# Kernel tuning notes

Measured on AMD Instinct MI355X. Metric: run time of the kernel, lower is better.

Reference implementation:

```python
import jax, jax.numpy as jnp
import numpy as np

BATCH = 1024
MAX_LEN = 200
MAX_K = 8
IN_U = 256
OUT_U = 256
ITERATION = 3
NEG_PAD = jnp.float32(-2.0**16 + 1)  # -65535, same as torch code


def squash(x):
    # NOTE: torch code sums over dim=1, which here is the capsule (max_K) axis.
    vec_sq_norm = jnp.sum(jnp.square(x), axis=1, keepdims=True)
    scale = vec_sq_norm / (1.0 + vec_sq_norm) / jnp.sqrt(vec_sq_norm + 1e-9)
    return scale * x


def setup_inputs() -> dict:
    key = jax.random.key(0)
    k1, k2, k3, k4 = jax.random.split(key, 4)
    low_capsule = jax.random.normal(k1, (BATCH, MAX_LEN, IN_U), dtype=jnp.float32)
    seq_len = jax.random.randint(k2, (BATCH, 1), 0, MAX_LEN)  # values < max_len per assert
    S_matrix = jax.random.normal(k3, (IN_U, OUT_U), dtype=jnp.float32)
    B_matrix = jax.random.normal(k4, (1, MAX_K, MAX_LEN), dtype=jnp.float32)
    return {"low_capsule": low_capsule, "S_matrix": S_matrix,
            "B_matrix": B_matrix, "seq_len": seq_len}


def reference(low_capsule, S_matrix, B_matrix, seq_len):
    # mask: [B,1,L], broadcasts against B_matrix [1,K,L] -> [B,K,L]
    mask = jnp.arange(MAX_LEN)[None, None, :] < seq_len[:, :, None]
    # loop-invariant projection (torch recomputes identically each iteration)
    low_new = jnp.einsum('ble,eo->blo', low_capsule, S_matrix)  # [B,L,O]
    Bm = B_matrix
    high = None
    for _ in range(ITERATION):
        logits = jnp.where(mask, Bm, NEG_PAD)          # [B,K,L]
        W = jax.nn.softmax(logits, axis=-1)            # [B,K,L]
        high = squash(jnp.einsum('bkl,blo->bko', W, low_new))  # [B,K,O]
        B_delta = jnp.sum(jnp.einsum('bko,blo->bkl', high, low_new),
                          axis=0, keepdims=True)       # [1,K,L]
        Bm = Bm + B_delta
    return high
```

## Files before the change

### kernel.cpp

```cpp
#include <hip/hip_runtime.h>

#define BATCH   1024
#define MAXLEN  200
#define KCAPS   8
#define INU     256
#define OUTU    256
#define NEGPAD  -65535.0f
#define HSTR    264

typedef _Float16 f16;
typedef _Float16 f16x8 __attribute__((ext_vector_type(8)));
typedef float    f32x4 __attribute__((ext_vector_type(4)));
typedef float    f32x2 __attribute__((ext_vector_type(2)));

__global__ void k_prep(const float* __restrict__ S, const float* __restrict__ Bm,
                       f16* __restrict__ Shi, f16* __restrict__ Slo,
                       f16* __restrict__ Thi, f16* __restrict__ Tlo,
                       float* __restrict__ Bcur) {
    int idx = blockIdx.x * 256 + threadIdx.x;
    if (idx < KCAPS * MAXLEN) Bcur[idx] = Bm[idx];
    int j    = idx & 7;
    int lane = (idx >> 3) & 63;
    int nf   = (idx >> 9) & 15;
    int ks   = idx >> 13;
    int k = ks * 32 + (lane >> 4) * 8 + j;
    int n = nf * 16 + (lane & 15);
    float vS = S[k * 256 + n];
    f16 hS = (f16)vS;
    Shi[idx] = hS;
    Slo[idx] = (f16)(vS - (float)hS);
    float vT = S[n * 256 + k];
    f16 hT = (f16)vT;
    Thi[idx] = hT;
    Tlo[idx] = (f16)(vT - (float)hT);
}

#define EFRAG(MF, ACC) do {                                                          \
    const int l_  = (MF) * 16 + r15;                                                 \
    const int lc_ = (l_ < MAXLEN) ? l_ : (MAXLEN - 1);                               \
    const float* ap_ = lb + (size_t)lc_ * INU + q * 8;                               \
    f32x4 va[8], vb[8];                                                              \
    _Pragma("unroll")                                                                \
    for (int ks = 0; ks < 8; ks++) {                                                 \
        va[ks] = *reinterpret_cast<const f32x4*>(ap_ + ks * 32);                     \
        vb[ks] = *reinterpret_cast<const f32x4*>(ap_ + ks * 32 + 4);                 \
    }                                                                                \
    _Pragma("unroll")                                                                \
    for (int ks = 0; ks < 8; ks++) {                                                 \
        const int ob_ = ks * 32 + q * 8;                                             \
        f32x4 h0 = *reinterpret_cast<const f32x4*>(&GH[r15 * HSTR + ob_]);           \
        f32x4 h1 = *reinterpret_cast<const f32x4*>(&GH[r15 * HSTR + ob_ + 4]);       \
        f16x8 bh, bl, ah, al;                                                        \
        _Pragma("unroll")                                                            \
        for (int j = 0; j < 4; j++) { f16 t = (f16)h0[j]; bh[j] = t; bl[j] = (f16)(h0[j] - (float)t); } \
        _Pragma("unroll")                                                            \
        for (int j = 0; j < 4; j++) { f16 t = (f16)h1[j]; bh[4+j] = t; bl[4+j] = (f16)(h1[j] - (float)t); } \
        _Pragma("unroll")                                                            \
        for (int j = 0; j < 4; j++) { f16 t = (f16)va[ks][j]; ah[j] = t; al[j] = (f16)(va[ks][j] - (float)t); } \
        _Pragma("unroll")                                                            \
        for (int j = 0; j < 4; j++) { f16 t = (f16)vb[ks][j]; ah[4+j] = t; al[4+j] = (f16)(vb[ks][j] - (float)t); } \
        ACC = __builtin_amdgcn_mfma_f32_16x16x32_f16(ah, bh, ACC, 0, 0, 0);          \
        ACC = __builtin_amdgcn_mfma_f32_16x16x32_f16(al, bh, ACC, 0, 0, 0);          \
        ACC = __builtin_amdgcn_mfma_f32_16x16x32_f16(ah, bl, ACC, 0, 0, 0);          \
    }                                                                                \
} while (0)

__global__ __launch_bounds__(512, 4) void k_G(const float* __restrict__ Bcur,
                                              const int*   __restrict__ seq_len,
                                              const float* __restrict__ low,
                                              const f16*   __restrict__ Shi,
                                              const f16*   __restrict__ Slo,
                                              const f16*   __restrict__ Thi,
                                              const f16*   __restrict__ Tlo,
                                              float*       __restrict__ partials,
                                              float*       __restrict__ out,
                                              int do_T) {
    __shared__ float Wl[KCAPS * MAXLEN];
    __shared__ float GH[16 * HSTR];
    __shared__ float Sl2[2 * KCAPS * 256];
    const int b   = blockIdx.x;
    const int tid = threadIdx.x;
    const int len = seq_len[b];

    for (int i = tid; i < KCAPS * MAXLEN; i += 512) Wl[i] = Bcur[i];
    for (int i = tid; i < 16 * HSTR; i += 512) GH[i] = 0.f;
    __syncthreads();

    {
        const int k  = tid >> 6;
        const int ln = tid & 63;
        float m = -3.4e38f;
        for (int l = ln; l < MAXLEN; l += 64) {
            float v = (l < len) ? Wl[k * MAXLEN + l] : NEGPAD;
            m = fmaxf(m, v);
        }
        #pragma unroll
        for (int off = 32; off >= 1; off >>= 1) m = fmaxf(m, __shfl_xor(m, off));
        float ssum = 0.f;
        for (int l = ln; l < MAXLEN; l += 64) {
            float v = (l < len) ? Wl[k * MAXLEN + l] : NEGPAD;
            ssum += __expf(v - m);
        }
        #pragma unroll
        for (int off = 32; off >= 1; off >>= 1) ssum += __shfl_xor(ssum, off);
        float inv = 1.f / ssum;
        for (int l = ln; l < MAXLEN; l += 64) {
            float v = (l < len) ? Wl[k * MAXLEN + l] : NEGPAD;
            Wl[k * MAXLEN + l] = __expf(v - m) * inv;
        }
    }
    __syncthreads();

    const float* lb = low + (size_t)b * (MAXLEN * INU);

    {
        const int cp = tid & 127;
        const int rg = tid >> 7;
        const int lim = (len == 0) ? MAXLEN : len;
        const float* cb = lb + cp * 2;
        f32x2 g[KCAPS];
        #pragma unroll
        for (int k = 0; k < KCAPS; k++) g[k] = (f32x2){0.f, 0.f};
        int l = rg;
        for (; l + 4 < lim; l += 8) {
            f32x2 va = *reinterpret_cast<const f32x2*>(cb + l * INU);
            f32x2 vb = *reinterpret_cast<const f32x2*>(cb + (l + 4) * INU);
            #pragma unroll
            for (int k = 0; k < KCAPS; k++) {
                float wa = Wl[k * MAXLEN + l];
                float wb = Wl[k * MAXLEN + l + 4];
                g[k][0] = fmaf(wa, va[0], g[k][0]);
                g[k][1] = fmaf(wa, va[1], g[k][1]);
                g[k][0] = fmaf(wb, vb[0], g[k][0]);
                g[k][1] = fmaf(wb, vb[1], g[k][1]);
            }
        }
        if (l < lim) {
            f32x2 va = *reinterpret_cast<const f32x2*>(cb + l * INU);
            #pragma unroll
            for (int k = 0; k < KCAPS; k++) {
                float wa = Wl[k * MAXLEN + l];
                g[k][0] = fmaf(wa, va[0], g[k][0]);
                g[k][1] = fmaf(wa, va[1], g[k][1]);
            }
        }
        if (rg >= 2) {
            #pragma unroll
            for (int k = 0; k < KCAPS; k++)
                *reinterpret_cast<f32x2*>(&Sl2[((rg - 2) * KCAPS + k) * 256 + cp * 2]) = g[k];
        }
        __syncthreads();
        if (rg == 1) {
            #pragma unroll
            for (int k = 0; k < KCAPS; k++) {
                f32x2 t = *reinterpret_cast<f32x2*>(&Sl2[(KCAPS + k) * 256 + cp * 2]);
                g[k][0] += t[0]; g[k][1] += t[1];
                *reinterpret_cast<f32x2*>(&Sl2[(KCAPS + k) * 256 + cp * 2]) = g[k];
            }
        } else if (rg == 0) {
            #pragma unroll
            for (int k = 0; k < KCAPS; k++) {
                f32x2 t = *reinterpret_cast<f32x2*>(&Sl2[k * 256 + cp * 2]);
                g[k][0] += t[0]; g[k][1] += t[1];
            }
        }
        __syncthreads();
        if (rg == 0) {
            #pragma unroll
            for (int k = 0; k < KCAPS; k++) {
                f32x2 t = *reinterpret_cast<f32x2*>(&Sl2[(KCAPS + k) * 256 + cp * 2]);
                GH[k * HSTR + cp * 2]     = g[k][0] + t[0];
                GH[k * HSTR + cp * 2 + 1] = g[k][1] + t[1];
            }
        }
    }
    __syncthreads();

    const int wv = tid >> 6, lane = tid & 63;
    const int r15 = lane & 15, q = lane >> 4;
    f32x4 aC[2];
    aC[0] = (f32x4){0.f, 0.f, 0.f, 0.f};
    aC[1] = (f32x4){0.f, 0.f, 0.f, 0.f};
    #pragma unroll
    for (int ks = 0; ks < 8; ks++) {
        const float* gp = &GH[r15 * HSTR + ks * 32 + q * 8];
        f32x4 a0 = *reinterpret_cast<const f32x4*>(gp);
        f32x4 a1 = *reinterpret_cast<const f32x4*>(gp + 4);
        f16x8 ah, al;
        #pragma unroll
        for (int j = 0; j < 4; j++) {
            f16 t = (f16)a0[j]; ah[j] = t; al[j] = (f16)(a0[j] - (float)t);
        }
        #pragma unroll
        for (int j = 0; j < 4; j++) {
            f16 t = (f16)a1[j]; ah[4 + j] = t; al[4 + j] = (f16)(a1[j] - (float)t);
        }
        #pragma unroll
        for (int i = 0; i < 2; i++) {
            const int nf = wv * 2 + i;
            f16x8 bh = *reinterpret_cast<const f16x8*>(Shi + (ks * 16 + nf) * 512 + lane * 8);
            f16x8 bl = *reinterpret_cast<const f16x8*>(Slo + (ks * 16 + nf) * 512 + lane * 8);
            aC[i] = __builtin_amdgcn_mfma_f32_16x16x32_f16(ah, bh, aC[i], 0, 0, 0);
            aC[i] = __builtin_amdgcn_mfma_f32_16x16x32_f16(al, bh, aC[i], 0, 0, 0);
            aC[i] = __builtin_amdgcn_mfma_f32_16x16x32_f16(ah, bl, aC[i], 0, 0, 0);
        }
    }
    float s0, s1;
    {
        float n0 = aC[0][0]*aC[0][0] + aC[0][1]*aC[0][1] + aC[0][2]*aC[0][2] + aC[0][3]*aC[0][3];
        float n1 = aC[1][0]*aC[1][0] + aC[1][1]*aC[1][1] + aC[1][2]*aC[1][2] + aC[1][3]*aC[1][3];
        n0 += __shfl_xor(n0, 16);
        n1 += __shfl_xor(n1, 16);
        s0 = n0 / (1.f + n0) * (1.f / sqrtf(n0 + 1e-9f));
        s1 = n1 / (1.f + n1) * (1.f / sqrtf(n1 + 1e-9f));
    }
    if (!do_T) {
        if (q < 2) {
            #pragma unroll
            for (int r = 0; r < 4; r++) {
                out[((size_t)b * KCAPS + q * 4 + r) * OUTU + (wv * 2 + 0) * 16 + r15] = s0 * aC[0][r];
                out[((size_t)b * KCAPS + q * 4 + r) * OUTU + (wv * 2 + 1) * 16 + r15] = s1 * aC[1][r];
            }
        }
        return;
    }
    __syncthreads();
    if (q < 2) {
        #pragma unroll
        for (int r = 0; r < 4; r++) {
            GH[(q * 4 + r) * HSTR + (wv * 2 + 0) * 16 + r15] = s0 * aC[0][r];
            GH[(q * 4 + r) * HSTR + (wv * 2 + 1) * 16 + r15] = s1 * aC[1][r];
        }
    }
    __syncthreads();

    f32x4 aD[2];
    aD[0] = (f32x4){0.f, 0.f, 0.f, 0.f};
    aD[1] = (f32x4){0.f, 0.f, 0.f, 0.f};
    #pragma unroll
    for (int ks = 0; ks < 8; ks++) {
        const float* hp = &GH[r15 * HSTR + ks * 32 + q * 8];
        f32x4 a0 = *reinterpret_cast<const f32x4*>(hp);
        f32x4 a1 = *reinterpret_cast<const f32x4*>(hp + 4);
        f16x8 ah, al;
        #pragma unroll
        for (int j = 0; j < 4; j++) {
            f16 t = (f16)a0[j]; ah[j] = t; al[j] = (f16)(a0[j] - (float)t);
        }
        #pragma unroll
        for (int j = 0; j < 4; j++) {
            f16 t = (f16)a1[j]; ah[4 + j] = t; al[4 + j] = (f16)(a1[j] - (float)t);
        }
        #pragma unroll
        for (int i = 0; i < 2; i++) {
            const int nf = wv * 2 + i;
            f16x8 bh = *reinterpret_cast<const f16x8*>(Thi + (ks * 16 + nf) * 512 + lane * 8);
            f16x8 bl = *reinterpret_cast<const f16x8*>(Tlo + (ks * 16 + nf) * 512 + lane * 8);
            aD[i] = __builtin_amdgcn_mfma_f32_16x16x32_f16(ah, bh, aD[i], 0, 0, 0);
            aD[i] = __builtin_amdgcn_mfma_f32_16x16x32_f16(al, bh, aD[i], 0, 0, 0);
            aD[i] = __builtin_amdgcn_mfma_f32_16x16x32_f16(ah, bl, aD[i], 0, 0, 0);
        }
    }
    __syncthreads();
    if (q < 2) {
        #pragma unroll
        for (int r = 0; r < 4; r++) {
            GH[(q * 4 + r) * HSTR + (wv * 2 + 0) * 16 + r15] = aD[0][r];
            GH[(q * 4 + r) * HSTR + (wv * 2 + 1) * 16 + r15] = aD[1][r];
        }
    }
    __syncthreads();

    f32x4 accA = (f32x4){0.f, 0.f, 0.f, 0.f};
    f32x4 accB = (f32x4){0.f, 0.f, 0.f, 0.f};
    EFRAG(wv, accA);
    if (wv < 5) EFRAG(wv + 8, accB);

    if (r15 < KCAPS) {
        const int kcol = r15;
        {
            const int lbase = wv * 16 + q * 4;
            #pragma unroll
            for (int r = 0; r < 4; r++)
                partials[(size_t)(kcol * MAXLEN + lbase + r) * BATCH + b] = accA[r];
        }
        if (wv < 5) {
            const int lbase = (wv + 8) * 16 + q * 4;
            #pragma unroll
            for (int r = 0; r < 4; r++) {
                const int l = lbase + r;
                if (l < MAXLEN)
                    partials[(size_t)(kcol * MAXLEN + l) * BATCH + b] = accB[r];
            }
        }
    }
}

__global__ __launch_bounds__(256) void k_update(const float* __restrict__ partials,
                                                float* __restrict__ Bcur) {
    __shared__ float red[256];
    const int i   = blockIdx.x;
    const int tid = threadIdx.x;
    float s = 0.f;
    #pragma unroll
    for (int j = 0; j < BATCH / 256; j++) s += partials[(size_t)i * BATCH + tid + j * 256];
    red[tid] = s;
    __syncthreads();
    for (int st = 128; st > 0; st >>= 1) {
        if (tid < st) red[tid] += red[tid + st];
        __syncthreads();
    }
    if (tid == 0) Bcur[i] += red[0];
}

extern "C" void kernel_launch(void* const* d_in, const int* in_sizes, int n_in,
                              void* d_out, int out_size, void* d_ws, size_t ws_size,
                              hipStream_t stream) {
    const float* low = (const float*)d_in[0];
    const float* S   = (const float*)d_in[1];
    const float* Bm  = (const float*)d_in[2];
    const int*   seq = (const int*)d_in[3];
    float* out = (float*)d_out;

    char* ws = (char*)d_ws;
    float* Bcur     = (float*)ws;
    float* partials = (float*)(ws + 6400);
    f16*   Shi      = (f16*)(ws + 6560000);
    f16*   Slo      = (f16*)(ws + 6691072);
    f16*   Thi      = (f16*)(ws + 6822144);
    f16*   Tlo      = (f16*)(ws + 6953216);

    k_prep<<<256, 256, 0, stream>>>(S, Bm, Shi, Slo, Thi, Tlo, Bcur);
    for (int it = 0; it < 3; it++) {
        int last = (it == 2);
        k_G<<<BATCH, 512, 0, stream>>>(Bcur, seq, low, Shi, Slo, Thi, Tlo,
                                       partials, out, last ? 0 : 1);
        if (!last) k_update<<<KCAPS * MAXLEN, 256, 0, stream>>>(partials, Bcur);
    }
}
```

Measured before the change: 227.7 us.

## Shrink k_G to 256 threads with four waves each covering more columns

Halves the k_G block from 512 to 256 threads, so each wave now handles four N-fragments in the S/T MFMA products and up to four L-fragments in the E stage. The weighted-sum stage is rewritten so each wave streams full rows as float4 with a software-prefetched next row, and partial sums are reduced through the GH shared buffer instead of a separate Sl2 array, which cuts shared memory. The EFRAG macro loads inputs in two halves to lower register pressure, and the cross-lane-group reduction is now done with shuffles. The intent is to raise occupancy and per-thread work while cutting LDS and barrier cost, at the price of fewer threads per block available to hide memory latency.

New measurement: 328.9 us. 1.44x slower.

```diff
diff --git a/kernel.cpp b/kernel.cpp
--- a/kernel.cpp
+++ b/kernel.cpp
@@ -11,7 +11,6 @@
 typedef _Float16 f16;
 typedef _Float16 f16x8 __attribute__((ext_vector_type(8)));
 typedef float    f32x4 __attribute__((ext_vector_type(4)));
-typedef float    f32x2 __attribute__((ext_vector_type(2)));
 
 __global__ void k_prep(const float* __restrict__ S, const float* __restrict__ Bm,
                        f16* __restrict__ Shi, f16* __restrict__ Slo,
@@ -39,33 +38,36 @@
     const int l_  = (MF) * 16 + r15;                                                 \
     const int lc_ = (l_ < MAXLEN) ? l_ : (MAXLEN - 1);                               \
     const float* ap_ = lb + (size_t)lc_ * INU + q * 8;                               \
-    f32x4 va[8], vb[8];                                                              \
     _Pragma("unroll")                                                                \
-    for (int ks = 0; ks < 8; ks++) {                                                 \
-        va[ks] = *reinterpret_cast<const f32x4*>(ap_ + ks * 32);                     \
-        vb[ks] = *reinterpret_cast<const f32x4*>(ap_ + ks * 32 + 4);                 \
-    }                                                                                \
-    _Pragma("unroll")                                                                \
-    for (int ks = 0; ks < 8; ks++) {                                                 \
-        const int ob_ = ks * 32 + q * 8;                                             \
-        f32x4 h0 = *reinterpret_cast<const f32x4*>(&GH[r15 * HSTR + ob_]);           \
-        f32x4 h1 = *reinterpret_cast<const f32x4*>(&GH[r15 * HSTR + ob_ + 4]);       \
-        f16x8 bh, bl, ah, al;                                                        \
+    for (int half = 0; half < 2; half++) {                                           \
+        f32x4 va[4], vb[4];                                                          \
         _Pragma("unroll")                                                            \
-        for (int j = 0; j < 4; j++) { f16 t = (f16)h0[j]; bh[j] = t; bl[j] = (f16)(h0[j] - (float)t); } \
+        for (int kk = 0; kk < 4; kk++) {                                             \
+            va[kk] = *reinterpret_cast<const f32x4*>(ap_ + (half * 4 + kk) * 32);    \
+            vb[kk] = *reinterpret_cast<const f32x4*>(ap_ + (half * 4 + kk) * 32 + 4);\
+        }                                                                            \
         _Pragma("unroll")                                                            \
-        for (int j = 0; j < 4; j++) { f16 t = (f16)h1[j]; bh[4+j] = t; bl[4+j] = (f16)(h1[j] - (float)t); } \
-        _Pragma("unroll")                                                            \
-        for (int j = 0; j < 4; j++) { f16 t = (f16)va[ks][j]; ah[j] = t; al[j] = (f16)(va[ks][j] - (float)t); } \
-        _Pragma("unroll")                                                            \
-        for (int j = 0; j < 4; j++) { f16 t = (f16)vb[ks][j]; ah[4+j] = t; al[4+j] = (f16)(vb[ks][j] - (float)t); } \
-        ACC = __builtin_amdgcn_mfma_f32_16x16x32_f16(ah, bh, ACC, 0, 0, 0);          \
-        ACC = __builtin_amdgcn_mfma_f32_16x16x32_f16(al, bh, ACC, 0, 0, 0);          \
-        ACC = __builtin_amdgcn_mfma_f32_16x16x32_f16(ah, bl, ACC, 0, 0, 0);          \
+        for (int kk = 0; kk < 4; kk++) {                                             \
+            const int ob_ = (half * 4 + kk) * 32 + q * 8;                            \
+            f32x4 h0 = *reinterpret_cast<const f32x4*>(&GH[r15 * HSTR + ob_]);       \
+            f32x4 h1 = *reinterpret_cast<const f32x4*>(&GH[r15 * HSTR + ob_ + 4]);   \
+            f16x8 bh, bl, ah, al;                                                    \
+            _Pragma("unroll")                                                        \
+            for (int j = 0; j < 4; j++) { f16 t = (f16)h0[j]; bh[j] = t; bl[j] = (f16)(h0[j] - (float)t); } \
+            _Pragma("unroll")                                                        \
+            for (int j = 0; j < 4; j++) { f16 t = (f16)h1[j]; bh[4+j] = t; bl[4+j] = (f16)(h1[j] - (float)t); } \
+            _Pragma("unroll")                                                        \
+            for (int j = 0; j < 4; j++) { f16 t = (f16)va[kk][j]; ah[j] = t; al[j] = (f16)(va[kk][j] - (float)t); } \
+            _Pragma("unroll")                                                        \
+            for (int j = 0; j < 4; j++) { f16 t = (f16)vb[kk][j]; ah[4+j] = t; al[4+j] = (f16)(vb[kk][j] - (float)t); } \
+            ACC = __builtin_amdgcn_mfma_f32_16x16x32_f16(ah, bh, ACC, 0, 0, 0);      \
+            ACC = __builtin_amdgcn_mfma_f32_16x16x32_f16(al, bh, ACC, 0, 0, 0);      \
+            ACC = __builtin_amdgcn_mfma_f32_16x16x32_f16(ah, bl, ACC, 0, 0, 0);      \
+        }                                                                            \
     }                                                                                \
 } while (0)
 
-__global__ __launch_bounds__(512, 4) void k_G(const float* __restrict__ Bcur,
+__global__ __launch_bounds__(256, 6) void k_G(const float* __restrict__ Bcur,
                                               const int*   __restrict__ seq_len,
                                               const float* __restrict__ low,
                                               const f16*   __restrict__ Shi,
@@ -77,34 +79,33 @@
                                               int do_T) {
     __shared__ float Wl[KCAPS * MAXLEN];
     __shared__ float GH[16 * HSTR];
-    __shared__ float Sl2[2 * KCAPS * 256];
     const int b   = blockIdx.x;
     const int tid = threadIdx.x;
     const int len = seq_len[b];
 
-    for (int i = tid; i < KCAPS * MAXLEN; i += 512) Wl[i] = Bcur[i];
-    for (int i = tid; i < 16 * HSTR; i += 512) GH[i] = 0.f;
+    for (int i = tid; i < KCAPS * MAXLEN; i += 256) Wl[i] = Bcur[i];
+    for (int i = tid; i < 16 * HSTR; i += 256) GH[i] = 0.f;
     __syncthreads();
 
     {
-        const int k  = tid >> 6;
-        const int ln = tid & 63;
+        const int k  = tid >> 5;
+        const int ln = tid & 31;
         float m = -3.4e38f;
-        for (int l = ln; l < MAXLEN; l += 64) {
+        for (int l = ln; l < MAXLEN; l += 32) {
             float v = (l < len) ? Wl[k * MAXLEN + l] : NEGPAD;
             m = fmaxf(m, v);
         }
         #pragma unroll
-        for (int off = 32; off >= 1; off >>= 1) m = fmaxf(m, __shfl_xor(m, off));
+        for (int off = 16; off >= 1; off >>= 1) m = fmaxf(m, __shfl_xor(m, off));
         float ssum = 0.f;
-        for (int l = ln; l < MAXLEN; l += 64) {
+        for (int l = ln; l < MAXLEN; l += 32) {
             float v = (l < len) ? Wl[k * MAXLEN + l] : NEGPAD;
             ssum += __expf(v - m);
         }
         #pragma unroll
-        for (int off = 32; off >= 1; off >>= 1) ssum += __shfl_xor(ssum, off);
+        for (int off = 16; off >= 1; off >>= 1) ssum += __shfl_xor(ssum, off);
         float inv = 1.f / ssum;
-        for (int l = ln; l < MAXLEN; l += 64) {
+        for (int l = ln; l < MAXLEN; l += 32) {
             float v = (l < len) ? Wl[k * MAXLEN + l] : NEGPAD;
             Wl[k * MAXLEN + l] = __expf(v - m) * inv;
         }
@@ -112,75 +113,55 @@
     __syncthreads();
 
     const float* lb = low + (size_t)b * (MAXLEN * INU);
-
-    {
-        const int cp = tid & 127;
-        const int rg = tid >> 7;
-        const int lim = (len == 0) ? MAXLEN : len;
-        const float* cb = lb + cp * 2;
-        f32x2 g[KCAPS];
-        #pragma unroll
-        for (int k = 0; k < KCAPS; k++) g[k] = (f32x2){0.f, 0.f};
-        int l = rg;
-        for (; l + 4 < lim; l += 8) {
-            f32x2 va = *reinterpret_cast<const f32x2*>(cb + l * INU);
-            f32x2 vb = *reinterpret_cast<const f32x2*>(cb + (l + 4) * INU);
-            #pragma unroll
-            for (int k = 0; k < KCAPS; k++) {
-                float wa = Wl[k * MAXLEN + l];
-                float wb = Wl[k * MAXLEN + l + 4];
-                g[k][0] = fmaf(wa, va[0], g[k][0]);
-                g[k][1] = fmaf(wa, va[1], g[k][1]);
-                g[k][0] = fmaf(wb, vb[0], g[k][0]);
-                g[k][1] = fmaf(wb, vb[1], g[k][1]);
-            }
-        }
-        if (l < lim) {
-            f32x2 va = *reinterpret_cast<const f32x2*>(cb + l * INU);
-            #pragma unroll
-            for (int k = 0; k < KCAPS; k++) {
-                float wa = Wl[k * MAXLEN + l];
-                g[k][0] = fmaf(wa, va[0], g[k][0]);
-                g[k][1] = fmaf(wa, va[1], g[k][1]);
-            }
-        }
-        if (rg >= 2) {
-            #pragma unroll
-            for (int k = 0; k < KCAPS; k++)
-                *reinterpret_cast<f32x2*>(&Sl2[((rg - 2) * KCAPS + k) * 256 + cp * 2]) = g[k];
-        }
-        __syncthreads();
-        if (rg == 1) {
-            #pragma unroll
-            for (int k = 0; k < KCAPS; k++) {
-                f32x2 t = *reinterpret_cast<f32x2*>(&Sl2[(KCAPS + k) * 256 + cp * 2]);
-                g[k][0] += t[0]; g[k][1] += t[1];
-                *reinterpret_cast<f32x2*>(&Sl2[(KCAPS + k) * 256 + cp * 2]) = g[k];
-            }
-        } else if (rg == 0) {
-            #pragma unroll
-            for (int k = 0; k < KCAPS; k++) {
-                f32x2 t = *reinterpret_cast<f32x2*>(&Sl2[k * 256 + cp * 2]);
-                g[k][0] += t[0]; g[k][1] += t[1];
-            }
-        }
-        __syncthreads();
-        if (rg == 0) {
-            #pragma unroll
-            for (int k = 0; k < KCAPS; k++) {
-                f32x2 t = *reinterpret_cast<f32x2*>(&Sl2[(KCAPS + k) * 256 + cp * 2]);
-                GH[k * HSTR + cp * 2]     = g[k][0] + t[0];
-                GH[k * HSTR + cp * 2 + 1] = g[k][1] + t[1];
-            }
-        }
-    }
-    __syncthreads();
-
     const int wv = tid >> 6, lane = tid & 63;
     const int r15 = lane & 15, q = lane >> 4;
-    f32x4 aC[2];
-    aC[0] = (f32x4){0.f, 0.f, 0.f, 0.f};
-    aC[1] = (f32x4){0.f, 0.f, 0.f, 0.f};
+
+    {
+        const int lim = (len == 0) ? MAXLEN : len;
+        f32x4 g[KCAPS];
+        #pragma unroll
+        for (int k = 0; k < KCAPS; k++) g[k] = (f32x4){0.f, 0.f, 0.f, 0.f};
+        int l = wv;
+        if (l < lim) {
+            f32x4 vcur = *reinterpret_cast<const f32x4*>(lb + l * INU + lane * 4);
+            for (;;) {
+                const int ln2 = l + 4;
+                const bool more = (ln2 < lim);
+                f32x4 vnext;
+                if (more) vnext = *reinterpret_cast<const f32x4*>(lb + ln2 * INU + lane * 4);
+                #pragma unroll
+                for (int k = 0; k < KCAPS; k++) {
+                    const float wa = Wl[k * MAXLEN + l];
+                    g[k][0] = fmaf(wa, vcur[0], g[k][0]);
+                    g[k][1] = fmaf(wa, vcur[1], g[k][1]);
+                    g[k][2] = fmaf(wa, vcur[2], g[k][2]);
+                    g[k][3] = fmaf(wa, vcur[3], g[k][3]);
+                }
+                if (!more) break;
+                l = ln2;
+                vcur = vnext;
+            }
+        }
+        if (wv >= 2) {
+            #pragma unroll
+            for (int k = 0; k < KCAPS; k++)
+                *reinterpret_cast<f32x4*>(&GH[((wv - 2) * 8 + k) * HSTR + lane * 4]) = g[k];
+        }
+        __syncthreads();
+        if (wv < 2) {
+            #pragma unroll
+            for (int k = 0; k < KCAPS; k++) {
+                float* p = &GH[(wv * 8 + k) * HSTR + lane * 4];
+                f32x4 t = *reinterpret_cast<const f32x4*>(p);
+                *reinterpret_cast<f32x4*>(p) = t + g[k];
+            }
+        }
+    }
+    __syncthreads();
+
+    f32x4 aC[4];
+    #pragma unroll
+    for (int i = 0; i < 4; i++) aC[i] = (f32x4){0.f, 0.f, 0.f, 0.f};
     #pragma unroll
     for (int ks = 0; ks < 8; ks++) {
         const float* gp = &GH[r15 * HSTR + ks * 32 + q * 8];
@@ -196,8 +177,8 @@
             f16 t = (f16)a1[j]; ah[4 + j] = t; al[4 + j] = (f16)(a1[j] - (float)t);
         }
         #pragma unroll
-        for (int i = 0; i < 2; i++) {
-            const int nf = wv * 2 + i;
+        for (int i = 0; i < 4; i++) {
+            const int nf = wv * 4 + i;
             f16x8 bh = *reinterpret_cast<const f16x8*>(Shi + (ks * 16 + nf) * 512 + lane * 8);
             f16x8 bl = *reinterpret_cast<const f16x8*>(Slo + (ks * 16 + nf) * 512 + lane * 8);
             aC[i] = __builtin_amdgcn_mfma_f32_16x16x32_f16(ah, bh, aC[i], 0, 0, 0);
@@ -205,38 +186,40 @@
             aC[i] = __builtin_amdgcn_mfma_f32_16x16x32_f16(ah, bl, aC[i], 0, 0, 0);
         }
     }
-    float s0, s1;
-    {
-        float n0 = aC[0][0]*aC[0][0] + aC[0][1]*aC[0][1] + aC[0][2]*aC[0][2] + aC[0][3]*aC[0][3];
-        float n1 = aC[1][0]*aC[1][0] + aC[1][1]*aC[1][1] + aC[1][2]*aC[1][2] + aC[1][3]*aC[1][3];
-        n0 += __shfl_xor(n0, 16);
-        n1 += __shfl_xor(n1, 16);
-        s0 = n0 / (1.f + n0) * (1.f / sqrtf(n0 + 1e-9f));
-        s1 = n1 / (1.f + n1) * (1.f / sqrtf(n1 + 1e-9f));
+    float s[4];
+    #pragma unroll
+    for (int i = 0; i < 4; i++) {
+        #pragma unroll
+        for (int r = 0; r < 4; r++) aC[i][r] += __shfl_xor(aC[i][r], 32);
+        float n = aC[i][0]*aC[i][0] + aC[i][1]*aC[i][1] + aC[i][2]*aC[i][2] + aC[i][3]*aC[i][3];
+        n += __shfl_xor(n, 16);
+        s[i] = n / (1.f + n) * (1.f / sqrtf(n + 1e-9f));
     }
     if (!do_T) {
         if (q < 2) {
             #pragma unroll
-            for (int r = 0; r < 4; r++) {
-                out[((size_t)b * KCAPS + q * 4 + r) * OUTU + (wv * 2 + 0) * 16 + r15] = s0 * aC[0][r];
-                out[((size_t)b * KCAPS + q * 4 + r) * OUTU + (wv * 2 + 1) * 16 + r15] = s1 * aC[1][r];
+            for (int i = 0; i < 4; i++) {
+                const int col = (wv * 4 + i) * 16 + r15;
+                #pragma unroll
+                for (int r = 0; r < 4; r++)
+                    out[((size_t)b * KCAPS + q * 4 + r) * OUTU + col] = s[i] * aC[i][r];
             }
         }
         return;
     }
     __syncthreads();
-    if (q < 2) {
-        #pragma unroll
-        for (int r = 0; r < 4; r++) {
-            GH[(q * 4 + r) * HSTR + (wv * 2 + 0) * 16 + r15] = s0 * aC[0][r];
-            GH[(q * 4 + r) * HSTR + (wv * 2 + 1) * 16 + r15] = s1 * aC[1][r];
-        }
-    }
-    __syncthreads();
-
-    f32x4 aD[2];
-    aD[0] = (f32x4){0.f, 0.f, 0.f, 0.f};
-    aD[1] = (f32x4){0.f, 0.f, 0.f, 0.f};
+    #pragma unroll
+    for (int i = 0; i < 4; i++) {
+        const int col = (wv * 4 + i) * 16 + r15;
+        #pragma unroll
+        for (int r = 0; r < 4; r++)
+            GH[(q * 4 + r) * HSTR + col] = (q < 2) ? s[i] * aC[i][r] : 0.f;
+    }
+    __syncthreads();
+
+    f32x4 aD[4];
+    #pragma unroll
+    for (int i = 0; i < 4; i++) aD[i] = (f32x4){0.f, 0.f, 0.f, 0.f};
     #pragma unroll
     for (int ks = 0; ks < 8; ks++) {
         const float* hp = &GH[r15 * HSTR + ks * 32 + q * 8];
@@ -252,8 +235,8 @@
             f16 t = (f16)a1[j]; ah[4 + j] = t; al[4 + j] = (f16)(a1[j] - (float)t);
         }
         #pragma unroll
-        for (int i = 0; i < 2; i++) {
-            const int nf = wv * 2 + i;
+        for (int i = 0; i < 4; i++) {
+            const int nf = wv * 4 + i;
             f16x8 bh = *reinterpret_cast<const f16x8*>(Thi + (ks * 16 + nf) * 512 + lane * 8);
             f16x8 bl = *reinterpret_cast<const f16x8*>(Tlo + (ks * 16 + nf) * 512 + lane * 8);
             aD[i] = __builtin_amdgcn_mfma_f32_16x16x32_f16(ah, bh, aD[i], 0, 0, 0);
@@ -262,19 +245,23 @@
         }
     }
     __syncthreads();
-    if (q < 2) {
-        #pragma unroll
-        for (int r = 0; r < 4; r++) {
-            GH[(q * 4 + r) * HSTR + (wv * 2 + 0) * 16 + r15] = aD[0][r];
-            GH[(q * 4 + r) * HSTR + (wv * 2 + 1) * 16 + r15] = aD[1][r];
-        }
+    #pragma unroll
+    for (int i = 0; i < 4; i++) {
+        const int col = (wv * 4 + i) * 16 + r15;
+        #pragma unroll
+        for (int r = 0; r < 4; r++)
+            GH[(q * 4 + r) * HSTR + col] = (q < 2) ? aD[i][r] : 0.f;
     }
     __syncthreads();
 
     f32x4 accA = (f32x4){0.f, 0.f, 0.f, 0.f};
     f32x4 accB = (f32x4){0.f, 0.f, 0.f, 0.f};
+    f32x4 accC = (f32x4){0.f, 0.f, 0.f, 0.f};
+    f32x4 accD = (f32x4){0.f, 0.f, 0.f, 0.f};
     EFRAG(wv, accA);
-    if (wv < 5) EFRAG(wv + 8, accB);
+    EFRAG(wv + 4, accB);
+    EFRAG(wv + 8, accC);
+    if (wv == 0) EFRAG(12, accD);
 
     if (r15 < KCAPS) {
         const int kcol = r15;
@@ -284,13 +271,25 @@
             for (int r = 0; r < 4; r++)
                 partials[(size_t)(kcol * MAXLEN + lbase + r) * BATCH + b] = accA[r];
         }
-        if (wv < 5) {
+        {
+            const int lbase = (wv + 4) * 16 + q * 4;
+            #pragma unroll
+            for (int r = 0; r < 4; r++)
+                partials[(size_t)(kcol * MAXLEN + lbase + r) * BATCH + b] = accB[r];
+        }
+        {
             const int lbase = (wv + 8) * 16 + q * 4;
+            #pragma unroll
+            for (int r = 0; r < 4; r++)
+                partials[(size_t)(kcol * MAXLEN + lbase + r) * BATCH + b] = accC[r];
+        }
+        if (wv == 0) {
+            const int lbase = 192 + q * 4;
             #pragma unroll
             for (int r = 0; r < 4; r++) {
                 const int l = lbase + r;
                 if (l < MAXLEN)
-                    partials[(size_t)(kcol * MAXLEN + l) * BATCH + b] = accB[r];
+                    partials[(size_t)(kcol * MAXLEN + l) * BATCH + b] = accD[r];
             }
         }
     }
@@ -333,7 +332,7 @@
     k_prep<<<256, 256, 0, stream>>>(S, Bm, Shi, Slo, Thi, Tlo, Bcur);
     for (int it = 0; it < 3; it++) {
         int last = (it == 2);
-        k_G<<<BATCH, 512, 0, stream>>>(Bcur, seq, low, Shi, Slo, Thi, Tlo,
+        k_G<<<BATCH, 256, 0, stream>>>(Bcur, seq, low, Shi, Slo, Thi, Tlo,
                                        partials, out, last ? 0 : 1);
         if (!last) k_update<<<KCAPS * MAXLEN, 256, 0, stream>>>(partials, Bcur);
     }
```
